# Optimization experiments

Measured on AMD Instinct MI355X. Metric: run time of the kernel, lower is better.

The kernel has to match this reference:

```python
import jax, jax.numpy as jnp
import numpy as np

STRIDE = 1
PAD = 3
DIL = 1


def setup_inputs() -> dict:
    key = jax.random.key(0)
    k1, k2, k3 = jax.random.split(key, 3)
    B, C, H, W = 8, 256, 64, 64
    G, K = 4, 7
    Ho, Wo = 64, 64  # same-padding, stride 1
    return {
        "input": jax.random.normal(k1, (B, C, H, W), dtype=jnp.float32),
        "weight": jax.random.normal(k2, (B, G, K, K, Ho, Wo), dtype=jnp.float32),
        "bias": jax.random.normal(k3, (C,), dtype=jnp.float32),
    }


def reference(input, weight, bias):
    # input: [B,C,H,W], weight: [B,G,Kh,Kw,Ho,Wo], bias: [C]
    B, C, H, W = input.shape
    G, Kh, Kw, Ho, Wo = weight.shape[1:]
    Cpg = C // G
    xp = jnp.pad(input, ((0, 0), (0, 0), (PAD, PAD), (PAD, PAD)))
    # group view: [B, G, C/G, H+2p, W+2p]
    xg = xp.reshape(B, G, Cpg, H + 2 * PAD, W + 2 * PAD)
    out = jnp.zeros((B, G, Cpg, Ho, Wo), dtype=input.dtype)
    # fused accumulation over the K*K kernel taps; no im2col blowup
    for kh in range(Kh):
        for kw in range(Kw):
            h0 = kh * DIL
            w0 = kw * DIL
            patch = xg[:, :, :, h0:h0 + Ho * STRIDE:STRIDE, w0:w0 + Wo * STRIDE:STRIDE]
            out = out + patch * weight[:, :, kh, kw][:, :, None, :, :]
    out = out.reshape(B, C, Ho, Wo) + bias[None, :, None, None]
    return out
```

## Files before the change

kernel.cpp:

```cpp
#include <hip/hip_runtime.h>


#define BLK_X 16
#define BLK_Y 8
#define NTHR (BLK_X * BLK_Y)
#define STG_ROWS 14
#define STG_COLS 70
#define STG_N (STG_ROWS * STG_COLS)
#define LDS_STRIDE 71
#define NSTG 8
#define CH_PER_BLK 16

__global__ __launch_bounds__(NTHR, 2)
void involution_kernel(const float* __restrict__ in,
                       const float* __restrict__ w,
                       const float* __restrict__ bias,
                       float* __restrict__ out) {
    __shared__ float lds[STG_ROWS * LDS_STRIDE];

    const int tx = threadIdx.x;
    const int ty = threadIdx.y;
    const int tid = ty * BLK_X + tx;
    const int x0 = tx * 4;
    const int Y0 = blockIdx.x * BLK_Y;
    const int y  = Y0 + ty;
    const int c0 = blockIdx.y * CH_PER_BLK;
    const int bz = blockIdx.z;
    const int g  = bz & 3;

    float4 w4[49];
    const float* wb = w + (size_t)bz * 49 * 4096 + y * 64 + x0;
    #pragma unroll
    for (int k = 0; k < 49; ++k) {
        w4[k] = *(const float4*)(wb + (size_t)k * 4096);
    }

    const float* inb  = in  + (size_t)bz * 64 * 4096;
    float*       outb = out + (size_t)bz * 64 * 4096;

    float stg[NSTG];

    auto load_c = [&](int c, float* r) {
        const float* p = inb + (size_t)c * 4096;
        #pragma unroll
        for (int j = 0; j < NSTG; ++j) {
            int i = tid + j * NTHR;
            float v = 0.f;
            if (i < STG_N) {
                int rr = i / STG_COLS;
                int cc = i - rr * STG_COLS;
                int gy = Y0 + rr - 3;
                int gx = cc - 3;
                if (gy >= 0 && gy < 64 && gx >= 0 && gx < 64)
                    v = p[gy * 64 + gx];
            }
            r[j] = v;
        }
    };
    auto write_stage = [&](const float* r) {
        #pragma unroll
        for (int j = 0; j < NSTG; ++j) {
            int i = tid + j * NTHR;
            if (i < STG_N) {
                int rr = i / STG_COLS;
                int cc = i - rr * STG_COLS;
                lds[rr * LDS_STRIDE + cc] = r[j];
            }
        }
    };

    load_c(c0, stg);
    write_stage(stg);
    __syncthreads();

    for (int cc = 0; cc < CH_PER_BLK; ++cc) {
        const int c = c0 + cc;

        float nstg[NSTG];
        if (cc + 1 < CH_PER_BLK) load_c(c + 1, nstg);

        float acc0 = 0.f, acc1 = 0.f, acc2 = 0.f, acc3 = 0.f;
        #pragma unroll
        for (int kh = 0; kh < 7; ++kh) {
            const float* lrow = &lds[(ty + kh) * LDS_STRIDE + x0];
            float vals[10];
            #pragma unroll
            for (int j = 0; j < 10; ++j) vals[j] = lrow[j];
            #pragma unroll
            for (int kw = 0; kw < 7; ++kw) {
                const float4 wv = w4[kh * 7 + kw];
                acc0 += vals[kw + 0] * wv.x;
                acc1 += vals[kw + 1] * wv.y;
                acc2 += vals[kw + 2] * wv.z;
                acc3 += vals[kw + 3] * wv.w;
            }
        }

        const float bv = bias[g * 64 + c];
        float4 o;
        o.x = acc0 + bv; o.y = acc1 + bv; o.z = acc2 + bv; o.w = acc3 + bv;
        *(float4*)(outb + (size_t)c * 4096 + y * 64 + x0) = o;

        if (cc + 1 < CH_PER_BLK) {
            __syncthreads();
            write_stage(nstg);
            __syncthreads();
        }
    }
}

extern "C" void kernel_launch(void* const* d_in, const int* in_sizes, int n_in,
                              void* d_out, int out_size, void* d_ws, size_t ws_size,
                              hipStream_t stream) {
    const float* in   = (const float*)d_in[0];
    const float* wgt  = (const float*)d_in[1];
    const float* bias = (const float*)d_in[2];
    float* out = (float*)d_out;

    dim3 block(BLK_X, BLK_Y, 1);
    dim3 grid(64 / BLK_Y, 64 / CH_PER_BLK, 32);
    involution_kernel<<<grid, block, 0, stream>>>(in, wgt, bias, out);
}
```

Before: 125.8 us.

## Restructure involution tiling: 4 channels per block, stream weights per kernel row

Blocks now cover 16 output rows with 256 threads and process 4 channels at once. All 4 channel tiles are staged into LDS together, which removes the per-channel double-buffer loop and its barriers. Weights are no longer held as 49 float4 registers; each kernel row's 7 float4s are loaded from global memory and reused across the 4 channels. This cuts register pressure so occupancy can be higher (launch bounds 4). The cost is that weights are re-read from global memory once per 4 channels instead of once per 16, and LDS rows are read with vector loads on a padded stride of 72.

```diff
diff --git a/kernel.cpp b/kernel.cpp
--- a/kernel.cpp
+++ b/kernel.cpp
@@ -2,110 +2,98 @@
 
 
 #define BLK_X 16
-#define BLK_Y 8
-#define NTHR (BLK_X * BLK_Y)
-#define STG_ROWS 14
-#define STG_COLS 70
-#define STG_N (STG_ROWS * STG_COLS)
-#define LDS_STRIDE 71
-#define NSTG 8
-#define CH_PER_BLK 16
+#define BLK_Y 16
+#define NTHR  256
+#define NC    4
+#define ROWS  16
+#define S_ROWS 22
+#define S_STRIDE 72
+#define S_CH (S_ROWS * S_STRIDE)
+#define S_ELEMS (S_ROWS * 70)
 
-__global__ __launch_bounds__(NTHR, 2)
+__global__ __launch_bounds__(NTHR, 4)
 void involution_kernel(const float* __restrict__ in,
                        const float* __restrict__ w,
                        const float* __restrict__ bias,
                        float* __restrict__ out) {
-    __shared__ float lds[STG_ROWS * LDS_STRIDE];
+    __shared__ float lds[NC * S_CH];
 
-    const int tx = threadIdx.x;
-    const int ty = threadIdx.y;
+    const int tx  = threadIdx.x;
+    const int ty  = threadIdx.y;
     const int tid = ty * BLK_X + tx;
-    const int x0 = tx * 4;
-    const int Y0 = blockIdx.x * BLK_Y;
-    const int y  = Y0 + ty;
-    const int c0 = blockIdx.y * CH_PER_BLK;
-    const int bz = blockIdx.z;
-    const int g  = bz & 3;
-
-    float4 w4[49];
-    const float* wb = w + (size_t)bz * 49 * 4096 + y * 64 + x0;
-    #pragma unroll
-    for (int k = 0; k < 49; ++k) {
-        w4[k] = *(const float4*)(wb + (size_t)k * 4096);
-    }
+    const int x0  = tx * 4;
+    const int Y0  = blockIdx.x * ROWS;
+    const int y   = Y0 + ty;
+    const int c0  = blockIdx.y * NC;
+    const int bz  = blockIdx.z;
+    const int g   = bz & 3;
 
     const float* inb  = in  + (size_t)bz * 64 * 4096;
     float*       outb = out + (size_t)bz * 64 * 4096;
+    const float* wb   = w   + (size_t)bz * 49 * 4096 + y * 64 + x0;
 
-    float stg[NSTG];
-
-    auto load_c = [&](int c, float* r) {
-        const float* p = inb + (size_t)c * 4096;
+    #pragma unroll
+    for (int c = 0; c < NC; ++c) {
+        const float* p = inb + (size_t)(c0 + c) * 4096;
+        float* l = lds + c * S_CH;
         #pragma unroll
-        for (int j = 0; j < NSTG; ++j) {
+        for (int j = 0; j < 7; ++j) {
             int i = tid + j * NTHR;
-            float v = 0.f;
-            if (i < STG_N) {
-                int rr = i / STG_COLS;
-                int cc = i - rr * STG_COLS;
-                int gy = Y0 + rr - 3;
-                int gx = cc - 3;
+            if (i < S_ELEMS) {
+                int r  = i / 70;
+                int cl = i - r * 70;
+                int gy = Y0 + r - 3;
+                int gx = cl - 3;
+                float v = 0.f;
                 if (gy >= 0 && gy < 64 && gx >= 0 && gx < 64)
                     v = p[gy * 64 + gx];
-            }
-            r[j] = v;
-        }
-    };
-    auto write_stage = [&](const float* r) {
-        #pragma unroll
-        for (int j = 0; j < NSTG; ++j) {
-            int i = tid + j * NTHR;
-            if (i < STG_N) {
-                int rr = i / STG_COLS;
-                int cc = i - rr * STG_COLS;
-                lds[rr * LDS_STRIDE + cc] = r[j];
+                l[r * S_STRIDE + cl] = v;
             }
         }
-    };
-
-    load_c(c0, stg);
-    write_stage(stg);
+    }
     __syncthreads();
 
-    for (int cc = 0; cc < CH_PER_BLK; ++cc) {
-        const int c = c0 + cc;
+    float acc[NC][4];
+    #pragma unroll
+    for (int c = 0; c < NC; ++c) {
+        acc[c][0] = 0.f; acc[c][1] = 0.f; acc[c][2] = 0.f; acc[c][3] = 0.f;
+    }
 
-        float nstg[NSTG];
-        if (cc + 1 < CH_PER_BLK) load_c(c + 1, nstg);
+    #pragma unroll 1
+    for (int kh = 0; kh < 7; ++kh) {
+        float4 wv[7];
+        #pragma unroll
+        for (int kw = 0; kw < 7; ++kw)
+            wv[kw] = *(const float4*)(wb + (size_t)(kh * 7 + kw) * 4096);
 
-        float acc0 = 0.f, acc1 = 0.f, acc2 = 0.f, acc3 = 0.f;
         #pragma unroll
-        for (int kh = 0; kh < 7; ++kh) {
-            const float* lrow = &lds[(ty + kh) * LDS_STRIDE + x0];
-            float vals[10];
-            #pragma unroll
-            for (int j = 0; j < 10; ++j) vals[j] = lrow[j];
+        for (int c = 0; c < NC; ++c) {
+            const float* lr = lds + c * S_CH + (ty + kh) * S_STRIDE + x0;
+            float4 va = *(const float4*)(lr);
+            float4 vb = *(const float4*)(lr + 4);
+            float2 vc = *(const float2*)(lr + 8);
+            float vals[10] = {va.x, va.y, va.z, va.w,
+                              vb.x, vb.y, vb.z, vb.w,
+                              vc.x, vc.y};
             #pragma unroll
             for (int kw = 0; kw < 7; ++kw) {
-                const float4 wv = w4[kh * 7 + kw];
-                acc0 += vals[kw + 0] * wv.x;
-                acc1 += vals[kw + 1] * wv.y;
-                acc2 += vals[kw + 2] * wv.z;
-                acc3 += vals[kw + 3] * wv.w;
+                acc[c][0] += vals[kw + 0] * wv[kw].x;
+                acc[c][1] += vals[kw + 1] * wv[kw].y;
+                acc[c][2] += vals[kw + 2] * wv[kw].z;
+                acc[c][3] += vals[kw + 3] * wv[kw].w;
             }
         }
+    }
 
-        const float bv = bias[g * 64 + c];
+    #pragma unroll
+    for (int c = 0; c < NC; ++c) {
+        const float bv = bias[g * 64 + c0 + c];
         float4 o;
-        o.x = acc0 + bv; o.y = acc1 + bv; o.z = acc2 + bv; o.w = acc3 + bv;
-        *(float4*)(outb + (size_t)c * 4096 + y * 64 + x0) = o;
-
-        if (cc + 1 < CH_PER_BLK) {
-            __syncthreads();
-            write_stage(nstg);
-            __syncthreads();
-        }
+        o.x = acc[c][0] + bv;
+        o.y = acc[c][1] + bv;
+        o.z = acc[c][2] + bv;
+        o.w = acc[c][3] + bv;
+        *(float4*)(outb + (size_t)(c0 + c) * 4096 + y * 64 + x0) = o;
     }
 }
 
@@ -118,6 +106,6 @@
     float* out = (float*)d_out;
 
     dim3 block(BLK_X, BLK_Y, 1);
-    dim3 grid(64 / BLK_Y, 64 / CH_PER_BLK, 32);
+    dim3 grid(64 / ROWS, 64 / NC, 32);
     involution_kernel<<<grid, block, 0, stream>>>(in, wgt, bias, out);
 }
```

Result: slower. 140.8 us (+11.9%).
